# Performance work log

Measured on AMD Instinct MI355X. Metric: run time of the kernel, lower is better.

Reference implementation:

```python
import jax, jax.numpy as jnp
import numpy as np

EMBED = 768
HEADS = 12


def setup_inputs() -> dict:
    key = jax.random.key(0)
    k1, k2, k3, k4, k5 = jax.random.split(key, 5)
    B, N, E = 8, 1024, EMBED
    x = jax.random.normal(k1, (B, N, E), dtype=jnp.float32)
    # torch Linear stored as [in, out] here (math-equivalent: y = x @ W + b)
    w_qkv = jax.random.normal(k2, (E, 3 * E), dtype=jnp.float32) * (E ** -0.5)
    b_qkv = jax.random.normal(k3, (3 * E,), dtype=jnp.float32) * 0.02
    w_proj = jax.random.normal(k4, (E, E), dtype=jnp.float32) * (E ** -0.5)
    b_proj = jax.random.normal(k5, (E,), dtype=jnp.float32) * 0.02
    return {"x": x, "w_qkv": w_qkv, "b_qkv": b_qkv, "w_proj": w_proj, "b_proj": b_proj}


def reference(x, w_qkv, b_qkv, w_proj, b_proj):
    B, N, E = x.shape
    H = HEADS
    D = E // H
    qkv = x @ w_qkv + b_qkv                       # [B, N, 3E]
    # rearrange 'b n (h d qkv) -> qkv b h n d': qkv index is innermost in last dim
    qkv = qkv.reshape(B, N, H, D, 3)
    qkv = jnp.transpose(qkv, (4, 0, 2, 1, 3))      # [3, B, H, N, D]
    q, k, v = qkv[0], qkv[1], qkv[2]
    energy = jnp.einsum('bhqd,bhkd->bhqk', q, k)   # [B, H, N, N]
    scaling = float(E) ** 0.5
    # NOTE: original scales AFTER softmax (unusual but faithful)
    att = jax.nn.softmax(energy, axis=-1) / scaling
    # dropout_prob = 0.0 -> identity
    out = jnp.einsum('bhqk,bhkd->bhqd', att, v)    # [B, H, N, D]
    out = jnp.transpose(out, (0, 2, 1, 3)).reshape(B, N, E)
    return out @ w_proj + b_proj
```

## Files before the change

kernel.cpp:

```cpp
#include <hip/hip_runtime.h>
#include <hip/hip_bf16.h>
#include <stdint.h>

#define NSEQ 1024
#define EMB 768
#define HEADS 12
#define HD 64
#define BATCH 8
#define BHN (BATCH*HEADS)

typedef __attribute__((ext_vector_type(8))) short bf16x8;
typedef __attribute__((ext_vector_type(4))) short bf16x4;
typedef __attribute__((ext_vector_type(4))) float f32x4;

typedef const void __attribute__((address_space(1))) cglobal_void;
typedef void __attribute__((address_space(3))) lds_void_t;

#define LOG2E 1.4426950408889634f

__device__ __forceinline__ void load_lds16(const void* g, void* l) {
    __builtin_amdgcn_global_load_lds((cglobal_void*)g, (lds_void_t*)l, 16, 0, 0);
}

__device__ __forceinline__ unsigned short f2bf(float f) {
    __hip_bfloat16 h = __float2bfloat16(f);
    return *reinterpret_cast<unsigned short*>(&h);
}

__device__ __forceinline__ unsigned int cvt_pk_bf16(float lo, float hi) {
    unsigned int r;
    asm("v_cvt_pk_bf16_f32 %0, %1, %2" : "=v"(r) : "v"(lo), "v"(hi));
    return r;
}

__device__ __forceinline__ float exp2_hw(float x) {
#if __has_builtin(__builtin_amdgcn_exp2f)
    return __builtin_amdgcn_exp2f(x);
#else
    return exp2f(x);
#endif
}

__global__ void conv_x_kernel(const float* __restrict__ x, unsigned short* __restrict__ xb) {
    int i = (blockIdx.x * 256 + threadIdx.x) * 4;
    float4 v = *reinterpret_cast<const float4*>(x + i);
    ushort4 o;
    o.x = f2bf(v.x); o.y = f2bf(v.y); o.z = f2bf(v.z); o.w = f2bf(v.w);
    *reinterpret_cast<ushort4*>(xb + i) = o;
}

template <int PERM>
__global__ void transpose_w_kernel(const float* __restrict__ w, unsigned short* __restrict__ wt,
                                   int K, int C) {
    __shared__ unsigned short tile[64][65];
    int c0 = blockIdx.x * 64;
    int k0 = blockIdx.y * 64;
    int t = threadIdx.x;
    int r = t >> 2, cc = (t & 3) * 16;
#pragma unroll
    for (int e = 0; e < 16; e += 4) {
        float4 v = *reinterpret_cast<const float4*>(w + (size_t)(k0 + r) * C + c0 + cc + e);
        float s0 = (PERM && ((c0 + cc + e + 0) % 3 == 0)) ? LOG2E : 1.0f;
        float s1 = (PERM && ((c0 + cc + e + 1) % 3 == 0)) ? LOG2E : 1.0f;
        float s2 = (PERM && ((c0 + cc + e + 2) % 3 == 0)) ? LOG2E : 1.0f;
        float s3 = (PERM && ((c0 + cc + e + 3) % 3 == 0)) ? LOG2E : 1.0f;
        tile[r][cc + e + 0] = f2bf(v.x * s0);
        tile[r][cc + e + 1] = f2bf(v.y * s1);
        tile[r][cc + e + 2] = f2bf(v.z * s2);
        tile[r][cc + e + 3] = f2bf(v.w * s3);
    }
    __syncthreads();
    int c = t >> 2, kk0 = (t & 3) * 16;
    int cg = c0 + c;
    int n;
    if (PERM) {
        int qkv = cg % 3, h = cg / 192, d = (cg % 192) / 3;
        n = qkv * EMB + h * HD + d;
    } else {
        n = cg;
    }
    uint4 lo, hi;
    lo.x = (unsigned)tile[kk0 + 0][c] | ((unsigned)tile[kk0 + 1][c] << 16);
    lo.y = (unsigned)tile[kk0 + 2][c] | ((unsigned)tile[kk0 + 3][c] << 16);
    lo.z = (unsigned)tile[kk0 + 4][c] | ((unsigned)tile[kk0 + 5][c] << 16);
    lo.w = (unsigned)tile[kk0 + 6][c] | ((unsigned)tile[kk0 + 7][c] << 16);
    hi.x = (unsigned)tile[kk0 + 8][c] | ((unsigned)tile[kk0 + 9][c] << 16);
    hi.y = (unsigned)tile[kk0 + 10][c] | ((unsigned)tile[kk0 + 11][c] << 16);
    hi.z = (unsigned)tile[kk0 + 12][c] | ((unsigned)tile[kk0 + 13][c] << 16);
    hi.w = (unsigned)tile[kk0 + 14][c] | ((unsigned)tile[kk0 + 15][c] << 16);
    *reinterpret_cast<uint4*>(wt + (size_t)n * K + k0 + kk0) = lo;
    *reinterpret_cast<uint4*>(wt + (size_t)n * K + k0 + kk0 + 8) = hi;
}

__global__ void perm_bias_kernel(const float* __restrict__ b, float* __restrict__ bp) {
    int c = blockIdx.x * 256 + threadIdx.x;
    int qkv = c % 3, h = c / 192, d = (c % 192) / 3;
    bp[qkv * EMB + h * HD + d] = (qkv == 0) ? b[c] * LOG2E : b[c];
}

__launch_bounds__(256, 4)
__global__ void gemm_qkv_kernel(const unsigned short* __restrict__ A,
                                const unsigned short* __restrict__ Bt,
                                const float* __restrict__ bias,
                                unsigned short* __restrict__ qout,
                                unsigned short* __restrict__ kout,
                                unsigned short* __restrict__ vout) {
    constexpr int TN = 18;
    constexpr int NWG = 64 * TN;
    constexpr int CHUNK = NWG / 8;
    constexpr int K = EMB;
    __shared__ unsigned short lds_a[128 * 64];
    __shared__ unsigned short lds_b[128 * 64];
    int bx0 = blockIdx.x;
    int bx = (bx0 % 8) * CHUNK + bx0 / 8;
    int tm = bx / TN, tn = bx % TN;
    bool vpath = (tn >= 12);
    const unsigned short* Bt_eff = Bt + (vpath ? (size_t)1536 * K : (size_t)0);
    const float* bias_eff = bias + (vpath ? 1536 : 0);
    int n0 = (vpath ? tn - 12 : tn) * 128;
    int m0 = tm * 128;
    int t = threadIdx.x;
    int l = t & 63;
    int g = l >> 4, c16 = l & 15;
    int wr = (t >> 7) & 1, wc = (t >> 6) & 1;
    int wbase = (t & 192);

    const char* baseA_f = vpath ? (const char*)lds_b : (const char*)lds_a;
    const char* baseB_f = vpath ? (const char*)lds_a : (const char*)lds_b;
    int roA = (vpath ? wc : wr) * 64;
    int roB = (vpath ? wr : wc) * 64;

    f32x4 acc[4][4];
#pragma unroll
    for (int i = 0; i < 4; i++)
#pragma unroll
        for (int j = 0; j < 4; j++)
#pragma unroll
            for (int r = 0; r < 4; r++) acc[i][j][r] = 0.f;

    for (int kt = 0; kt < K; kt += 64) {
        __syncthreads();
#pragma unroll
        for (int i = 0; i < 4; i++) {
            int c = i * 256 + t;
            int row = c >> 3;
            int sc = ((c & 7) ^ (row & 7)) * 8;
            load_lds16(A + (size_t)(m0 + row) * K + kt + sc, lds_a + (size_t)(i * 256 + wbase) * 8);
            load_lds16(Bt_eff + (size_t)(n0 + row) * K + kt + sc, lds_b + (size_t)(i * 256 + wbase) * 8);
        }
        __syncthreads();
#pragma unroll
        for (int kk = 0; kk < 2; kk++) {
            int cb = kk * 64 + g * 16;
            bf16x8 fa[4], fb[4];
#pragma unroll
            for (int i = 0; i < 4; i++) {
                int row = roA + i * 16 + c16;
                fa[i] = *reinterpret_cast<const bf16x8*>(
                    baseA_f + row * 128 + (cb ^ ((row & 7) << 4)));
            }
#pragma unroll
            for (int j = 0; j < 4; j++) {
                int row = roB + j * 16 + c16;
                fb[j] = *reinterpret_cast<const bf16x8*>(
                    baseB_f + row * 128 + (cb ^ ((row & 7) << 4)));
            }
#pragma unroll
            for (int i = 0; i < 4; i++)
#pragma unroll
                for (int j = 0; j < 4; j++)
                    acc[i][j] = __builtin_amdgcn_mfma_f32_16x16x32_bf16(fa[i], fb[j], acc[i][j], 0, 0, 0);
        }
    }

    if (vpath) {
#pragma unroll
        for (int i = 0; i < 4; i++) {
#pragma unroll
            for (int r = 0; r < 4; r++) {
                int nv = wc * 64 + i * 16 + (g * 4) + r + n0;
                float bv = bias_eff[nv];
                int hh = nv >> 6, dd = nv & 63;
#pragma unroll
                for (int j = 0; j < 4; j++) {
                    int m_g = m0 + wr * 64 + j * 16 + c16;
                    int bb = m_g >> 10, nn = m_g & 1023;
                    int nnp = (nn & ~31) | ((nn & 12) << 1) | ((nn >> 2) & 4) | (nn & 3);
                    vout[((size_t)(bb * HEADS + hh) * HD + dd) * NSEQ + nnp] =
                        f2bf(acc[i][j][r] + bv);
                }
            }
        }
    } else {
#pragma unroll
        for (int i = 0; i < 4; i++) {
            int mbase = m0 + wr * 64 + i * 16 + (g * 4);
#pragma unroll
            for (int j = 0; j < 4; j++) {
                int n_g = n0 + wc * 64 + j * 16 + c16;
                float bv = bias_eff[n_g];
#pragma unroll
                for (int r = 0; r < 4; r++) {
                    int m_g = mbase + r;
                    float v = acc[i][j][r] + bv;
                    int rem = n_g - ((n_g >= 768) ? 768 : 0);
                    int hh = rem >> 6, dd = rem & 63;
                    int bb = m_g >> 10, nn = m_g & 1023;
                    if (n_g < 768)
                        qout[(size_t)((bb * HEADS + hh) * NSEQ + nn) * HD + dd] = f2bf(v);
                    else
                        kout[(size_t)((bb * HEADS + hh) * NSEQ + nn) * HD + dd] = f2bf(v);
                }
            }
        }
    }
}

__launch_bounds__(256, 4)
__global__ void proj_kernel(const unsigned short* __restrict__ A,
                            const unsigned short* __restrict__ Bt,
                            const float* __restrict__ bias,
                            float* __restrict__ out) {
    constexpr int TN = 6;
    constexpr int NWG = 128 * TN;
    constexpr int CHUNK = NWG / 8;
    constexpr int K = EMB;
    __shared__ unsigned short lds_a[64 * 64];
    __shared__ unsigned short lds_b[128 * 64];
    int bx0 = blockIdx.x;
    int bx = (bx0 % 8) * CHUNK + bx0 / 8;
    int tm = bx / TN, tn = bx % TN;
    int m0 = tm * 64, n0 = tn * 128;
    int t = threadIdx.x;
    int l = t & 63;
    int g = l >> 4, c16 = l & 15;
    int w = t >> 6;
    int wbase = (t & 192);

    f32x4 acc[4][2];
#pragma unroll
    for (int i = 0; i < 4; i++)
#pragma unroll
        for (int j = 0; j < 2; j++)
#pragma unroll
            for (int r = 0; r < 4; r++) acc[i][j][r] = 0.f;

    for (int kt = 0; kt < K; kt += 64) {
        __syncthreads();
#pragma unroll
        for (int i = 0; i < 2; i++) {
            int c = i * 256 + t;
            int row = c >> 3;
            int sc = ((c & 7) ^ (row & 7)) * 8;
            load_lds16(A + (size_t)(m0 + row) * K + kt + sc, lds_a + (size_t)(i * 256 + wbase) * 8);
        }
#pragma unroll
        for (int i = 0; i < 4; i++) {
            int c = i * 256 + t;
            int row = c >> 3;
            int sc = ((c & 7) ^ (row & 7)) * 8;
            load_lds16(Bt + (size_t)(n0 + row) * K + kt + sc, lds_b + (size_t)(i * 256 + wbase) * 8);
        }
        __syncthreads();
#pragma unroll
        for (int kk = 0; kk < 2; kk++) {
            int cb = kk * 64 + g * 16;
            bf16x8 fa[4], fb[2];
#pragma unroll
            for (int i = 0; i < 4; i++) {
                int row = i * 16 + c16;
                fa[i] = *reinterpret_cast<const bf16x8*>(
                    (const char*)lds_a + row * 128 + (cb ^ ((row & 7) << 4)));
            }
#pragma unroll
            for (int j = 0; j < 2; j++) {
                int row = w * 32 + j * 16 + c16;
                fb[j] = *reinterpret_cast<const bf16x8*>(
                    (const char*)lds_b + row * 128 + (cb ^ ((row & 7) << 4)));
            }
#pragma unroll
            for (int i = 0; i < 4; i++)
#pragma unroll
                for (int j = 0; j < 2; j++)
                    acc[i][j] = __builtin_amdgcn_mfma_f32_16x16x32_bf16(fa[i], fb[j], acc[i][j], 0, 0, 0);
        }
    }

#pragma unroll
    for (int i = 0; i < 4; i++) {
        int mbase = m0 + i * 16 + g * 4;
#pragma unroll
        for (int j = 0; j < 2; j++) {
            int n_g = n0 + w * 32 + j * 16 + c16;
            float bv = bias[n_g];
#pragma unroll
            for (int r = 0; r < 4; r++)
                out[(size_t)(mbase + r) * EMB + n_g] = acc[i][j][r] + bv;
        }
    }
}

__launch_bounds__(256, 3)
__global__ void attn_kernel(const unsigned short* __restrict__ Q,
                            const unsigned short* __restrict__ K,
                            const unsigned short* __restrict__ Vt,
                            unsigned short* __restrict__ Oout) {
    __shared__ unsigned short k_lds[2][64 * 64];
    __shared__ unsigned short vt_lds[2][64 * 64];
    int bx = blockIdx.x;
    int bh = bx % BHN;
    int q0 = (bx / BHN) << 7;
    int b = bh / HEADS, h = bh % HEADS;
    int t = threadIdx.x, w = t >> 6, l = t & 63;
    int g = l >> 4, c16 = l & 15;
    const unsigned short* Qh = Q + (size_t)bh * NSEQ * HD;
    const unsigned short* Kh = K + (size_t)bh * NSEQ * HD;
    const unsigned short* Vth = Vt + (size_t)bh * NSEQ * HD;

    int qrA = q0 + w * 32 + c16;
    int qrB = qrA + 16;
    bf16x8 qfA[2], qfB[2];
    qfA[0] = *reinterpret_cast<const bf16x8*>(Qh + (size_t)qrA * HD + g * 8);
    qfA[1] = *reinterpret_cast<const bf16x8*>(Qh + (size_t)qrA * HD + 32 + g * 8);
    qfB[0] = *reinterpret_cast<const bf16x8*>(Qh + (size_t)qrB * HD + g * 8);
    qfB[1] = *reinterpret_cast<const bf16x8*>(Qh + (size_t)qrB * HD + 32 + g * 8);

    float lA = 0.f, lB = 0.f;
    f32x4 accA[4], accB[4];
#pragma unroll
    for (int jd = 0; jd < 4; jd++)
#pragma unroll
        for (int r = 0; r < 4; r++) { accA[jd][r] = 0.f; accB[jd][r] = 0.f; }

    auto stage = [&](int buf, int kv) {
#pragma unroll
        for (int i = 0; i < 2; i++) {
            int tt = i * 256 + t;
            int row = tt >> 3;
            int sc = ((tt & 7) ^ (row & 7)) * 8;
            load_lds16(Kh + (size_t)(kv + row) * HD + sc, k_lds[buf] + (size_t)(tt & ~63) * 8);
            load_lds16(Vth + (size_t)row * NSEQ + kv + sc, vt_lds[buf] + (size_t)(tt & ~63) * 8);
        }
    };

    stage(0, 0);
    __syncthreads();
    int cur = 0;
    for (int it = 0; it < 16; ++it) {
        if (it < 15) stage(cur ^ 1, (it + 1) << 6);

        const char* kbase = (const char*)k_lds[cur];
        const char* vbase = (const char*)vt_lds[cur];

        f32x4 stA[4], stB[4];
#pragma unroll
        for (int jk = 0; jk < 4; jk++)
#pragma unroll
            for (int r = 0; r < 4; r++) { stA[jk][r] = 0.f; stB[jk][r] = 0.f; }
        __builtin_amdgcn_s_setprio(1);
#pragma unroll
        for (int kk = 0; kk < 2; kk++) {
            int cb = kk * 64 + g * 16;
#pragma unroll
            for (int jk = 0; jk < 4; jk++) {
                int row = jk * 16 + c16;
                bf16x8 kf = *reinterpret_cast<const bf16x8*>(
                    kbase + row * 128 + (cb ^ ((row & 7) << 4)));
                stA[jk] = __builtin_amdgcn_mfma_f32_16x16x32_bf16(kf, qfA[kk], stA[jk], 0, 0, 0);
                stB[jk] = __builtin_amdgcn_mfma_f32_16x16x32_bf16(kf, qfB[kk], stB[jk], 0, 0, 0);
            }
        }
        __builtin_amdgcn_s_setprio(0);

#pragma unroll
        for (int jk = 0; jk < 4; jk++)
#pragma unroll
            for (int r = 0; r < 4; r++) {
                stA[jk][r] = exp2_hw(stA[jk][r]);
                stB[jk][r] = exp2_hw(stB[jk][r]);
            }

        union PU { unsigned int u[4]; bf16x8 v; };
        PU puA0, puA1, puB0, puB1;
#pragma unroll
        for (int p = 0; p < 2; p++) {
            puA0.u[p]     = cvt_pk_bf16(stA[0][2 * p], stA[0][2 * p + 1]);
            puA0.u[2 + p] = cvt_pk_bf16(stA[1][2 * p], stA[1][2 * p + 1]);
            puA1.u[p]     = cvt_pk_bf16(stA[2][2 * p], stA[2][2 * p + 1]);
            puA1.u[2 + p] = cvt_pk_bf16(stA[3][2 * p], stA[3][2 * p + 1]);
            puB0.u[p]     = cvt_pk_bf16(stB[0][2 * p], stB[0][2 * p + 1]);
            puB0.u[2 + p] = cvt_pk_bf16(stB[1][2 * p], stB[1][2 * p + 1]);
            puB1.u[p]     = cvt_pk_bf16(stB[2][2 * p], stB[2][2 * p + 1]);
            puB1.u[2 + p] = cvt_pk_bf16(stB[3][2 * p], stB[3][2 * p + 1]);
        }
        bf16x8 pfA[2] = {puA0.v, puA1.v};
        bf16x8 pfB[2] = {puB0.v, puB1.v};

        __builtin_amdgcn_s_setprio(1);
#pragma unroll
        for (int ks = 0; ks < 2; ks++) {
            int cb = ks * 64 + g * 16;
#pragma unroll
            for (int jd = 0; jd < 4; jd++) {
                int row = jd * 16 + c16;
                bf16x8 vf = *reinterpret_cast<const bf16x8*>(
                    vbase + row * 128 + (cb ^ ((row & 7) << 4)));
                accA[jd] = __builtin_amdgcn_mfma_f32_16x16x32_bf16(vf, pfA[ks], accA[jd], 0, 0, 0);
                accB[jd] = __builtin_amdgcn_mfma_f32_16x16x32_bf16(vf, pfB[ks], accB[jd], 0, 0, 0);
            }
        }
        __builtin_amdgcn_s_setprio(0);

        lA += (((stA[0][0] + stA[0][1]) + (stA[0][2] + stA[0][3])) +
               ((stA[1][0] + stA[1][1]) + (stA[1][2] + stA[1][3]))) +
              (((stA[2][0] + stA[2][1]) + (stA[2][2] + stA[2][3])) +
               ((stA[3][0] + stA[3][1]) + (stA[3][2] + stA[3][3])));
        lB += (((stB[0][0] + stB[0][1]) + (stB[0][2] + stB[0][3])) +
               ((stB[1][0] + stB[1][1]) + (stB[1][2] + stB[1][3]))) +
              (((stB[2][0] + stB[2][1]) + (stB[2][2] + stB[2][3])) +
               ((stB[3][0] + stB[3][1]) + (stB[3][2] + stB[3][3])));

        __syncthreads();
        cur ^= 1;
    }

    lA += __shfl_xor(lA, 16);
    lA += __shfl_xor(lA, 32);
    lB += __shfl_xor(lB, 16);
    lB += __shfl_xor(lB, 32);
    const float scale = 27.712812921102035f;
    float invA = 1.0f / (lA * scale);
    float invB = 1.0f / (lB * scale);
    size_t qbaseA = ((size_t)(b * NSEQ + qrA) * HEADS + h) * HD;
    size_t qbaseB = ((size_t)(b * NSEQ + qrB) * HEADS + h) * HD;
#pragma unroll
    for (int jd = 0; jd < 4; jd++)
#pragma unroll
        for (int r = 0; r < 4; r++) {
            int d = jd * 16 + g * 4 + r;
            Oout[qbaseA + d] = f2bf(accA[jd][r] * invA);
            Oout[qbaseB + d] = f2bf(accB[jd][r] * invB);
        }
}

extern "C" void kernel_launch(void* const* d_in, const int* in_sizes, int n_in,
                              void* d_out, int out_size, void* d_ws, size_t ws_size,
                              hipStream_t stream) {
    const float* x = (const float*)d_in[0];
    const float* w_qkv = (const float*)d_in[1];
    const float* b_qkv = (const float*)d_in[2];
    const float* w_proj = (const float*)d_in[3];
    const float* b_proj = (const float*)d_in[4];

    char* ws = (char*)d_ws;
    unsigned short* xb      = (unsigned short*)(ws + 0);
    unsigned short* wt_qkv  = (unsigned short*)(ws + 12582912);
    unsigned short* wt_proj = (unsigned short*)(ws + 16121856);
    float*          biasp   = (float*)(ws + 17301504);
    unsigned short* qb      = (unsigned short*)(ws + 17310720);
    unsigned short* kb      = (unsigned short*)(ws + 29893632);
    unsigned short* vtb     = (unsigned short*)(ws + 42476544);
    unsigned short* ao      = (unsigned short*)(ws + 55059456);

    conv_x_kernel<<<6144, 256, 0, stream>>>(x, xb);
    transpose_w_kernel<1><<<dim3(36, 12), 256, 0, stream>>>(w_qkv, wt_qkv, EMB, 3 * EMB);
    transpose_w_kernel<0><<<dim3(12, 12), 256, 0, stream>>>(w_proj, wt_proj, EMB, EMB);
    perm_bias_kernel<<<9, 256, 0, stream>>>(b_qkv, biasp);

    gemm_qkv_kernel<<<64 * 18, 256, 0, stream>>>(xb, wt_qkv, biasp, qb, kb, vtb);
    attn_kernel<<<BHN * 8, 256, 0, stream>>>(qb, kb, vtb, ao);
    proj_kernel<<<128 * 6, 256, 0, stream>>>(ao, wt_proj, b_proj, (float*)d_out);
}
```

Before: 103.7 us.

## Software-pipeline attention loop so QK of next tile overlaps PV of previous

Restructures the attention inner loop into a one-stage software pipeline. Each iteration issues the QK^T MFMAs for the current KV tile and the PV MFMAs for the previous tile's probabilities back to back, then runs exp and pack. This lets the exp/convert work and the MFMA chains interleave better. It adds a third V^T LDS buffer, a prologue and an epilogue, and uses `#pragma unroll 1`, so register pressure and LDS use go up and may reduce occupancy.

After: 101.9 us. No clear change (-1.7%).

```diff
diff --git a/kernel.cpp b/kernel.cpp
--- a/kernel.cpp
+++ b/kernel.cpp
@@ -306,7 +306,7 @@
                             const unsigned short* __restrict__ Vt,
                             unsigned short* __restrict__ Oout) {
     __shared__ unsigned short k_lds[2][64 * 64];
-    __shared__ unsigned short vt_lds[2][64 * 64];
+    __shared__ unsigned short vt_lds[3][64 * 64];
     int bx = blockIdx.x;
     int bh = bx % BHN;
     int q0 = (bx / BHN) << 7;
@@ -332,46 +332,20 @@
 #pragma unroll
         for (int r = 0; r < 4; r++) { accA[jd][r] = 0.f; accB[jd][r] = 0.f; }
 
-    auto stage = [&](int buf, int kv) {
+    auto stage = [&](unsigned short* kdst, unsigned short* vdst, int kv) {
 #pragma unroll
         for (int i = 0; i < 2; i++) {
             int tt = i * 256 + t;
             int row = tt >> 3;
             int sc = ((tt & 7) ^ (row & 7)) * 8;
-            load_lds16(Kh + (size_t)(kv + row) * HD + sc, k_lds[buf] + (size_t)(tt & ~63) * 8);
-            load_lds16(Vth + (size_t)row * NSEQ + kv + sc, vt_lds[buf] + (size_t)(tt & ~63) * 8);
+            load_lds16(Kh + (size_t)(kv + row) * HD + sc, kdst + (size_t)(tt & ~63) * 8);
+            load_lds16(Vth + (size_t)row * NSEQ + kv + sc, vdst + (size_t)(tt & ~63) * 8);
         }
     };
 
-    stage(0, 0);
-    __syncthreads();
-    int cur = 0;
-    for (int it = 0; it < 16; ++it) {
-        if (it < 15) stage(cur ^ 1, (it + 1) << 6);
-
-        const char* kbase = (const char*)k_lds[cur];
-        const char* vbase = (const char*)vt_lds[cur];
-
-        f32x4 stA[4], stB[4];
-#pragma unroll
-        for (int jk = 0; jk < 4; jk++)
-#pragma unroll
-            for (int r = 0; r < 4; r++) { stA[jk][r] = 0.f; stB[jk][r] = 0.f; }
-        __builtin_amdgcn_s_setprio(1);
-#pragma unroll
-        for (int kk = 0; kk < 2; kk++) {
-            int cb = kk * 64 + g * 16;
-#pragma unroll
-            for (int jk = 0; jk < 4; jk++) {
-                int row = jk * 16 + c16;
-                bf16x8 kf = *reinterpret_cast<const bf16x8*>(
-                    kbase + row * 128 + (cb ^ ((row & 7) << 4)));
-                stA[jk] = __builtin_amdgcn_mfma_f32_16x16x32_bf16(kf, qfA[kk], stA[jk], 0, 0, 0);
-                stB[jk] = __builtin_amdgcn_mfma_f32_16x16x32_bf16(kf, qfB[kk], stB[jk], 0, 0, 0);
-            }
-        }
-        __builtin_amdgcn_s_setprio(0);
-
+    union PU { unsigned int u[4]; bf16x8 v; };
+    bf16x8 pfA[2], pfB[2];
+    auto softmax_pack = [&](f32x4 (&stA)[4], f32x4 (&stB)[4]) {
 #pragma unroll
         for (int jk = 0; jk < 4; jk++)
 #pragma unroll
@@ -379,8 +353,6 @@
                 stA[jk][r] = exp2_hw(stA[jk][r]);
                 stB[jk][r] = exp2_hw(stB[jk][r]);
             }
-
-        union PU { unsigned int u[4]; bf16x8 v; };
         PU puA0, puA1, puB0, puB1;
 #pragma unroll
         for (int p = 0; p < 2; p++) {
@@ -393,24 +365,8 @@
             puB1.u[p]     = cvt_pk_bf16(stB[2][2 * p], stB[2][2 * p + 1]);
             puB1.u[2 + p] = cvt_pk_bf16(stB[3][2 * p], stB[3][2 * p + 1]);
         }
-        bf16x8 pfA[2] = {puA0.v, puA1.v};
-        bf16x8 pfB[2] = {puB0.v, puB1.v};
-
-        __builtin_amdgcn_s_setprio(1);
-#pragma unroll
-        for (int ks = 0; ks < 2; ks++) {
-            int cb = ks * 64 + g * 16;
-#pragma unroll
-            for (int jd = 0; jd < 4; jd++) {
-                int row = jd * 16 + c16;
-                bf16x8 vf = *reinterpret_cast<const bf16x8*>(
-                    vbase + row * 128 + (cb ^ ((row & 7) << 4)));
-                accA[jd] = __builtin_amdgcn_mfma_f32_16x16x32_bf16(vf, pfA[ks], accA[jd], 0, 0, 0);
-                accB[jd] = __builtin_amdgcn_mfma_f32_16x16x32_bf16(vf, pfB[ks], accB[jd], 0, 0, 0);
-            }
-        }
-        __builtin_amdgcn_s_setprio(0);
-
+        pfA[0] = puA0.v; pfA[1] = puA1.v;
+        pfB[0] = puB0.v; pfB[1] = puB1.v;
         lA += (((stA[0][0] + stA[0][1]) + (stA[0][2] + stA[0][3])) +
                ((stA[1][0] + stA[1][1]) + (stA[1][2] + stA[1][3]))) +
               (((stA[2][0] + stA[2][1]) + (stA[2][2] + stA[2][3])) +
@@ -419,10 +375,83 @@
                ((stB[1][0] + stB[1][1]) + (stB[1][2] + stB[1][3]))) +
               (((stB[2][0] + stB[2][1]) + (stB[2][2] + stB[2][3])) +
                ((stB[3][0] + stB[3][1]) + (stB[3][2] + stB[3][3])));
-
+    };
+
+    auto qk_cluster = [&](const char* kbase, f32x4 (&stA)[4], f32x4 (&stB)[4]) {
+#pragma unroll
+        for (int kk = 0; kk < 2; kk++) {
+            int cb = kk * 64 + g * 16;
+#pragma unroll
+            for (int jk = 0; jk < 4; jk++) {
+                int row = jk * 16 + c16;
+                bf16x8 kf = *reinterpret_cast<const bf16x8*>(
+                    kbase + row * 128 + (cb ^ ((row & 7) << 4)));
+                stA[jk] = __builtin_amdgcn_mfma_f32_16x16x32_bf16(kf, qfA[kk], stA[jk], 0, 0, 0);
+                stB[jk] = __builtin_amdgcn_mfma_f32_16x16x32_bf16(kf, qfB[kk], stB[jk], 0, 0, 0);
+            }
+        }
+    };
+    auto pv_cluster = [&](const char* vbase) {
+#pragma unroll
+        for (int ks = 0; ks < 2; ks++) {
+            int cb = ks * 64 + g * 16;
+#pragma unroll
+            for (int jd = 0; jd < 4; jd++) {
+                int row = jd * 16 + c16;
+                bf16x8 vf = *reinterpret_cast<const bf16x8*>(
+                    vbase + row * 128 + (cb ^ ((row & 7) << 4)));
+                accA[jd] = __builtin_amdgcn_mfma_f32_16x16x32_bf16(vf, pfA[ks], accA[jd], 0, 0, 0);
+                accB[jd] = __builtin_amdgcn_mfma_f32_16x16x32_bf16(vf, pfB[ks], accB[jd], 0, 0, 0);
+            }
+        }
+    };
+
+    unsigned short* kcur = k_lds[0];
+    unsigned short* knxt = k_lds[1];
+    unsigned short* vprev = vt_lds[2];
+    unsigned short* vcur  = vt_lds[0];
+    unsigned short* vnxt  = vt_lds[1];
+
+    stage(kcur, vcur, 0);
+    __syncthreads();
+
+    {
+        stage(knxt, vnxt, 64);
+        f32x4 stA[4], stB[4];
+#pragma unroll
+        for (int jk = 0; jk < 4; jk++)
+#pragma unroll
+            for (int r = 0; r < 4; r++) { stA[jk][r] = 0.f; stB[jk][r] = 0.f; }
+        __builtin_amdgcn_s_setprio(1);
+        qk_cluster((const char*)kcur, stA, stB);
+        __builtin_amdgcn_s_setprio(0);
+        softmax_pack(stA, stB);
         __syncthreads();
-        cur ^= 1;
-    }
+        unsigned short* tmp = kcur; kcur = knxt; knxt = tmp;
+        unsigned short* tv = vprev; vprev = vcur; vcur = vnxt; vnxt = tv;
+    }
+
+#pragma unroll 1
+    for (int it = 1; it < 16; ++it) {
+        if (it < 15) stage(knxt, vnxt, (it + 1) << 6);
+        f32x4 stA[4], stB[4];
+#pragma unroll
+        for (int jk = 0; jk < 4; jk++)
+#pragma unroll
+            for (int r = 0; r < 4; r++) { stA[jk][r] = 0.f; stB[jk][r] = 0.f; }
+        __builtin_amdgcn_s_setprio(1);
+        qk_cluster((const char*)kcur, stA, stB);
+        pv_cluster((const char*)vprev);
+        __builtin_amdgcn_s_setprio(0);
+        softmax_pack(stA, stB);
+        __syncthreads();
+        unsigned short* tmp = kcur; kcur = knxt; knxt = tmp;
+        unsigned short* tv = vprev; vprev = vcur; vcur = vnxt; vnxt = tv;
+    }
+
+    __builtin_amdgcn_s_setprio(1);
+    pv_cluster((const char*)vprev);
+    __builtin_amdgcn_s_setprio(0);
 
     lA += __shfl_xor(lA, 16);
     lA += __shfl_xor(lA, 32);
```
